# Kernel optimization log

Hardware: AMD Instinct MI355X
Metric: run time of the kernel (lower is better)

## Reference

```python
import jax, jax.numpy as jnp
import numpy as np

B, N_V, N_H, K = 16384, 4096, 1024, 3
LR, MOMENTUM, WEIGHT_DECAY = 1e-3, 0.5, 1e-4


def setup_inputs() -> dict:
    key = jax.random.key(0)
    k1, k2, k3, k4 = jax.random.split(key, 4)
    inputs = jax.random.uniform(k1, (B, N_V), dtype=jnp.float32)
    weights = jax.random.normal(k2, (N_V, N_H), dtype=jnp.float32) * 0.1
    visible_bias = jnp.ones((N_V,), jnp.float32) * 0.5
    hidden_bias = jnp.zeros((N_H,), jnp.float32)
    weights_momentum = jnp.zeros((N_V, N_H), jnp.float32)
    visible_bias_momentum = jnp.zeros((N_V,), jnp.float32)
    hidden_bias_momentum = jnp.zeros((N_H,), jnp.float32)
    # one uniform vector of length n_hidden per sampling step (matches torch code)
    rand_h0 = jax.random.uniform(k3, (N_H,), dtype=jnp.float32)
    rand_hk = jax.random.uniform(k4, (K, N_H), dtype=jnp.float32)
    return {
        "inputs": inputs,
        "weights": weights,
        "visible_bias": visible_bias,
        "hidden_bias": hidden_bias,
        "weights_momentum": weights_momentum,
        "visible_bias_momentum": visible_bias_momentum,
        "hidden_bias_momentum": hidden_bias_momentum,
        "rand_h0": rand_h0,
        "rand_hk": rand_hk,
    }


def reference(inputs, weights, visible_bias, hidden_bias,
              weights_momentum, visible_bias_momentum, hidden_bias_momentum,
              rand_h0, rand_hk):
    dtype = inputs.dtype

    def sample_hidden(v):  # [B,V] -> [B,H]
        return jax.nn.sigmoid(v @ weights + hidden_bias)

    def sample_visible(h):  # [B,H] -> [B,V]
        return jax.nn.sigmoid(h @ weights.T + visible_bias)

    # positive phase
    pos_hidden_probs = sample_hidden(inputs)                      # [B,H]
    pos_hidden_acts = (pos_hidden_probs >= rand_h0).astype(dtype)  # [B,H]
    pos_associations = inputs.T @ pos_hidden_acts                 # [V,H]

    # negative phase (CD-k). NOTE: in the original torch code `hid_acts` is
    # never updated inside the k-1 loop, so every iteration recomputes the
    # identical visible_probs/hidden_probs from pos_hidden_acts; the extra
    # bernoulli draws (rand_hk) only feed hidden_acts, which is discarded.
    # The final values are therefore exactly one reconstruction step:
    neg_visible_probs = sample_visible(pos_hidden_acts)           # [B,V]
    neg_hidden_probs = sample_hidden(neg_visible_probs)           # [B,H]
    neg_associations = neg_visible_probs.T @ neg_hidden_probs     # [V,H]

    # momentum optimizer step
    batch_size = inputs.shape[0]
    w_mom = weights_momentum * MOMENTUM + (pos_associations - neg_associations)
    vb_mom = visible_bias_momentum * MOMENTUM + jnp.sum(inputs - neg_visible_probs, axis=0)
    hb_mom = hidden_bias_momentum * MOMENTUM + jnp.sum(pos_hidden_probs - neg_hidden_probs, axis=0)

    new_weights = weights + w_mom * (LR / batch_size)
    new_weights = new_weights - new_weights * WEIGHT_DECAY
    new_visible_bias = visible_bias + vb_mom * (LR / batch_size)
    new_hidden_bias = hidden_bias + hb_mom * (LR / batch_size)

    # reconstruction error (original has a bug using builtin `input`; intended `inputs`)
    error = jnp.sum((inputs - neg_visible_probs) ** 2)
    return (error, new_weights, new_visible_bias, new_hidden_bias)
```

## Files before the change

kernel.cpp:

```cpp
#include <hip/hip_runtime.h>
#include <hip/hip_bf16.h>

#define DEV __device__ __forceinline__

typedef __attribute__((ext_vector_type(8))) short bhalf8;
typedef __attribute__((ext_vector_type(4))) short bhalf4;
typedef __attribute__((ext_vector_type(4))) float floatx4;
typedef unsigned short ushort_t;

constexpr int NB = 16384;
constexpr int NV = 4096;
constexpr int NH = 1024;
constexpr float MOM = 0.5f;
constexpr float WD  = 1e-4f;
constexpr float LRB = 1e-3f / 16384.0f;

constexpr int LDS_SHORTS = 65536;
constexpr size_t LDS_BYTES = 131136;

DEV unsigned short f2bf(float f) {
  unsigned u = __builtin_bit_cast(unsigned, f);
  u += 0x7FFFu + ((u >> 16) & 1u);
  return (unsigned short)(u >> 16);
}
DEV float bf2f(unsigned short u) {
  unsigned x = ((unsigned)u) << 16;
  return __builtin_bit_cast(float, x);
}
DEV float sigm(float x) { return 1.0f / (1.0f + __expf(-x)); }

DEV void gl16(const ushort_t* g, ushort_t* l) {
  __builtin_amdgcn_global_load_lds(
      (const __attribute__((address_space(1))) void*)g,
      (__attribute__((address_space(3))) void*)l,
      16, 0, 0);
}

__global__ void prep_cvt_t(const float* __restrict__ in,
                           ushort_t* __restrict__ obf,
                           ushort_t* __restrict__ oT, int R, int C) {
  __shared__ ushort_t t[64][72];
  const int c0 = blockIdx.x * 64, r0 = blockIdx.y * 64;
  const int tr = threadIdx.x >> 3, tc = (threadIdx.x & 7) * 8;
#pragma unroll
  for (int s = 0; s < 64; s += 32) {
    const float* p = in + (size_t)(r0 + tr + s) * C + c0 + tc;
    floatx4 lo = *(const floatx4*)p, hi = *(const floatx4*)(p + 4);
    bhalf8 r;
    r[0] = (short)f2bf(lo[0]); r[1] = (short)f2bf(lo[1]);
    r[2] = (short)f2bf(lo[2]); r[3] = (short)f2bf(lo[3]);
    r[4] = (short)f2bf(hi[0]); r[5] = (short)f2bf(hi[1]);
    r[6] = (short)f2bf(hi[2]); r[7] = (short)f2bf(hi[3]);
    *(bhalf8*)(obf + (size_t)(r0 + tr + s) * C + c0 + tc) = r;
    *(bhalf8*)&t[tr + s][tc] = r;
  }
  __syncthreads();
#pragma unroll
  for (int s = 0; s < 64; s += 32) {
    bhalf8 v;
#pragma unroll
    for (int j = 0; j < 8; ++j) v[j] = (short)t[tc + j][tr + s];
    *(bhalf8*)(oT + (size_t)(c0 + tr + s) * R + r0 + tc) = v;
  }
}

DEV void core256(const ushort_t* __restrict__ Ap,
                 const ushort_t* __restrict__ Bp,
                 size_t ldA, size_t ldB, int NP,
                 ushort_t* Lp, int wid, int lane,
                 int wr, int wc, floatx4 (&acc)[8][4]) {
  const int lr = lane & 15, kg = lane >> 4;
  const int srow = wid * 16 + (lane >> 2);
  const int scol = (lane & 3) * 8;
  const ushort_t* gA = Ap + (size_t)srow * ldA + scol;
  const ushort_t* gB = Bp + (size_t)srow * ldB + scol;
  ushort_t* dA = Lp + wid * 512;
  ushort_t* dB = Lp + 8192 + wid * 512;
  const ushort_t* aB = Lp + (wr * 128 + lr) * 32 + kg * 8;
  const ushort_t* bB = Lp + 8192 + (wc * 64 + lr) * 32 + kg * 8;

  auto stage = [&](int p) {
    const int slot = (p & 3) * 16384;
    const size_t kb = (size_t)p * 32;
#pragma unroll
    for (int i = 0; i < 2; ++i) {
      gl16(gA + (size_t)(i * 128) * ldA + kb, dA + slot + i * 4096);
      gl16(gB + (size_t)(i * 128) * ldB + kb, dB + slot + i * 4096);
    }
  };

  stage(0); stage(1); stage(2);
  asm volatile("s_waitcnt vmcnt(8)" ::: "memory");
  asm volatile("s_barrier" ::: "memory");

  for (int p = 0; p < NP; ++p) {
    const int slot = (p & 3) * 16384;
    bhalf8 fa[4], fb[4], fa2[4];
#pragma unroll
    for (int i = 0; i < 4; ++i) fa[i] = *(const bhalf8*)(aB + slot + i * 512);
#pragma unroll
    for (int i = 0; i < 4; ++i) fb[i] = *(const bhalf8*)(bB + slot + i * 512);
    if (p + 3 < NP) stage(p + 3);
    asm volatile("s_barrier" ::: "memory");
    asm volatile("s_waitcnt lgkmcnt(0)" ::: "memory");
    __builtin_amdgcn_sched_barrier(0);
    __builtin_amdgcn_s_setprio(1);
#pragma unroll
    for (int m2 = 0; m2 < 4; ++m2)
#pragma unroll
      for (int n = 0; n < 4; ++n)
        acc[m2][n] = __builtin_amdgcn_mfma_f32_16x16x32_bf16(fa[m2], fb[n], acc[m2][n], 0, 0, 0);
    __builtin_amdgcn_s_setprio(0);
    asm volatile("s_barrier" ::: "memory");
#pragma unroll
    for (int i = 0; i < 4; ++i) fa2[i] = *(const bhalf8*)(aB + slot + 2048 + i * 512);
    asm volatile("s_barrier" ::: "memory");
    asm volatile("s_waitcnt lgkmcnt(0)" ::: "memory");
    __builtin_amdgcn_sched_barrier(0);
    __builtin_amdgcn_s_setprio(1);
#pragma unroll
    for (int m2 = 0; m2 < 4; ++m2)
#pragma unroll
      for (int n = 0; n < 4; ++n)
        acc[4 + m2][n] = __builtin_amdgcn_mfma_f32_16x16x32_bf16(fa2[m2], fb[n], acc[4 + m2][n], 0, 0, 0);
    __builtin_amdgcn_s_setprio(0);
    if (p + 3 < NP)      asm volatile("s_waitcnt vmcnt(8)" ::: "memory");
    else if (p + 2 < NP) asm volatile("s_waitcnt vmcnt(4)" ::: "memory");
    else if (p + 1 < NP) asm volatile("s_waitcnt vmcnt(0)" ::: "memory");
    asm volatile("s_barrier" ::: "memory");
  }
}

template <int MODE>
__global__ __launch_bounds__(512, 2)
void gemm_fused256(const ushort_t* __restrict__ Ab,
                   const ushort_t* __restrict__ Bb,
                   int N, int K,
                   const float* __restrict__ bias,
                   const float* __restrict__ rand_h0,
                   ushort_t* __restrict__ Pout,
                   ushort_t* __restrict__ PoutT,
                   float* __restrict__ colsum,
                   const ushort_t* __restrict__ inbf,
                   float* __restrict__ err_accum) {
  extern __shared__ ushort_t Lsh[];
  const int tid = threadIdx.x;
  const int wid = tid >> 6, lane = tid & 63;
  const int wr = wid >> 2, wc = wid & 3;
  const int lr = lane & 15, kg = lane >> 4;

  const int nwg = gridDim.x * gridDim.y;
  const int id = blockIdx.y * gridDim.x + blockIdx.x;
  const int sid = (id & 7) * (nwg >> 3) + (id >> 3);
  const int n0 = (sid % gridDim.x) * 256;
  const int m0 = (sid / gridDim.x) * 256;

  floatx4 acc[8][4] = {};
  core256(Ab + (size_t)m0 * K, Bb + (size_t)n0 * K, K, K, K / 32,
          Lsh, wid, lane, wr, wc, acc);

  float esum = 0.0f;
#pragma unroll
  for (int ni = 0; ni < 4; ++ni) {
    const int col = n0 + wc * 64 + ni * 16 + lr;
    const float b = bias[col];
    const float r0 = (MODE == 0) ? rand_h0[col] : 0.0f;
    float cs = 0.0f;
#pragma unroll
    for (int mi = 0; mi < 8; ++mi) {
      const int rowb = m0 + wr * 128 + mi * 16 + kg * 4;
      bhalf4 tp;
#pragma unroll
      for (int r = 0; r < 4; ++r) {
        const float p = sigm(acc[mi][ni][r] + b);
        ushort_t ov;
        if (MODE == 0) {
          cs += p;
          ov = (p >= r0) ? (ushort_t)0x3F80u : (ushort_t)0u;
          Pout[(size_t)(rowb + r) * N + col] = ov;
        } else if (MODE == 1) {
          ov = f2bf(p);
          Pout[(size_t)(rowb + r) * N + col] = ov;
          const float d = bf2f(inbf[(size_t)(rowb + r) * N + col]) - p;
          cs += d;
          esum += d * d;
        } else {
          cs += p;
          ov = f2bf(p);
        }
        tp[r] = (short)ov;
      }
      *(bhalf4*)&PoutT[(size_t)col * NB + rowb] = tp;
    }
    cs += __shfl_xor(cs, 16);
    cs += __shfl_xor(cs, 32);
    if (kg == 0) atomicAdd(&colsum[col], cs);
  }
  if (MODE == 1) {
    float* ered = (float*)(Lsh + LDS_SHORTS);
    esum += __shfl_xor(esum, 1);
    esum += __shfl_xor(esum, 2);
    esum += __shfl_xor(esum, 4);
    esum += __shfl_xor(esum, 8);
    esum += __shfl_xor(esum, 16);
    esum += __shfl_xor(esum, 32);
    if (lane == 0) ered[wid] = esum;
    __syncthreads();
    if (tid == 0) {
      float s = 0.0f;
#pragma unroll
      for (int w = 0; w < 8; ++w) s += ered[w];
      atomicAdd(err_accum, s);
    }
  }
}

template <int EOP>
__global__ __launch_bounds__(512, 2)
void gemm_nt256(const ushort_t* __restrict__ Ab,
                const ushort_t* __restrict__ Bb,
                int Ng, int ld, int ksp, float* __restrict__ outd) {
  extern __shared__ ushort_t Lsh[];
  const int tid = threadIdx.x;
  const int wid = tid >> 6, lane = tid & 63;
  const int wr = wid >> 2, wc = wid & 3;
  const int lr = lane & 15, kg = lane >> 4;

  const int nwg = gridDim.x * gridDim.y;
  const int id = blockIdx.y * gridDim.x + blockIdx.x;
  const int sid = (id & 7) * (nwg >> 3) + (id >> 3);
  const int n0 = (sid % gridDim.x) * 256;
  const int m0 = (sid / gridDim.x) * 256;
  const size_t kb0 = (size_t)blockIdx.z * ksp;

  floatx4 acc[8][4] = {};
  core256(Ab + (size_t)m0 * ld + kb0, Bb + (size_t)n0 * ld + kb0, ld, ld, ksp / 32,
          Lsh, wid, lane, wr, wc, acc);

  float* od = outd + (size_t)blockIdx.z * (size_t)gridDim.y * 256 * Ng;
#pragma unroll
  for (int mi = 0; mi < 8; ++mi) {
    const int rowb = m0 + wr * 128 + mi * 16 + kg * 4;
#pragma unroll
    for (int ni = 0; ni < 4; ++ni) {
      const int col = n0 + wc * 64 + ni * 16 + lr;
#pragma unroll
      for (int r = 0; r < 4; ++r) {
        float* p = &od[(size_t)(rowb + r) * Ng + col];
        if (EOP == 0) *p = acc[mi][ni][r];
        else          *p -= acc[mi][ni][r];
      }
    }
  }
}

__global__ void wupdate_kernel(const float* __restrict__ W, const float* __restrict__ wm,
                               const float* __restrict__ diff, float* __restrict__ outW) {
  const int i = blockIdx.x * blockDim.x + threadIdx.x;
  constexpr size_t SL = (size_t)NV * NH / 4;
  const floatx4 w = ((const floatx4*)W)[i];
  const floatx4 m = ((const floatx4*)wm)[i];
  const floatx4 a = ((const floatx4*)diff)[i];
  const floatx4 b = ((const floatx4*)diff)[i + SL];
  const floatx4 c = ((const floatx4*)diff)[i + 2 * SL];
  const floatx4 d = ((const floatx4*)diff)[i + 3 * SL];
  floatx4 o;
#pragma unroll
  for (int j = 0; j < 4; ++j)
    o[j] = (w[j] + (m[j] * MOM + (a[j] + b[j]) + (c[j] + d[j])) * LRB) * (1.0f - WD);
  ((floatx4*)outW)[i] = o;
}

__global__ void biaserr_kernel(const float* __restrict__ vb, const float* __restrict__ vbm,
                               const float* __restrict__ vbcs,
                               const float* __restrict__ hb, const float* __restrict__ hbm,
                               const float* __restrict__ phpcs, const float* __restrict__ nhpcs,
                               const float* __restrict__ err, float* __restrict__ out) {
  const int i = blockIdx.x * blockDim.x + threadIdx.x;
  if (i < NV) out[1 + (size_t)NV * NH + i] = vb[i] + (vbm[i] * MOM + vbcs[i]) * LRB;
  if (i < NH) out[1 + (size_t)NV * NH + NV + i] = hb[i] + (hbm[i] * MOM + (phpcs[i] - nhpcs[i])) * LRB;
  if (i == 0) out[0] = err[0];
}

extern "C" void kernel_launch(void* const* d_in, const int* in_sizes, int n_in,
                              void* d_out, int out_size, void* d_ws, size_t ws_size,
                              hipStream_t stream) {
  const float* inputs  = (const float*)d_in[0];
  const float* W       = (const float*)d_in[1];
  const float* vb      = (const float*)d_in[2];
  const float* hb      = (const float*)d_in[3];
  const float* wmom    = (const float*)d_in[4];
  const float* vbmom   = (const float*)d_in[5];
  const float* hbmom   = (const float*)d_in[6];
  const float* rand_h0 = (const float*)d_in[7];

  hipFuncSetAttribute((const void*)gemm_fused256<0>, hipFuncAttributeMaxDynamicSharedMemorySize, (int)LDS_BYTES);
  hipFuncSetAttribute((const void*)gemm_fused256<1>, hipFuncAttributeMaxDynamicSharedMemorySize, (int)LDS_BYTES);
  hipFuncSetAttribute((const void*)gemm_fused256<2>, hipFuncAttributeMaxDynamicSharedMemorySize, (int)LDS_BYTES);
  hipFuncSetAttribute((const void*)gemm_nt256<0>, hipFuncAttributeMaxDynamicSharedMemorySize, (int)LDS_BYTES);
  hipFuncSetAttribute((const void*)gemm_nt256<1>, hipFuncAttributeMaxDynamicSharedMemorySize, (int)LDS_BYTES);

  char* ws = (char*)d_ws;
  size_t off = 0;
  auto take = [&](size_t b) { size_t r = off; off = (off + b + 1023) & ~(size_t)1023; return r; };
  ushort_t* Wbf   = (ushort_t*)(ws + take((size_t)NV * NH * 2));
  ushort_t* WT    = (ushort_t*)(ws + take((size_t)NV * NH * 2));
  ushort_t* inbf  = (ushort_t*)(ws + take((size_t)NB * NV * 2));
  ushort_t* inT   = (ushort_t*)(ws + take((size_t)NB * NV * 2));
  ushort_t* nvp   = (ushort_t*)(ws + take((size_t)NB * NV * 2));
  ushort_t* nvpT  = (ushort_t*)(ws + take((size_t)NB * NV * 2));
  ushort_t* acts  = (ushort_t*)(ws + take((size_t)NB * NH * 2));
  ushort_t* actsT = (ushort_t*)(ws + take((size_t)NB * NH * 2));
  ushort_t* nhpT  = (ushort_t*)(ws + take((size_t)NB * NH * 2));
  const size_t red_bytes = (size_t)(NH + NH + NV + 64) * 4;
  float* phpcs = (float*)(ws + take(red_bytes));
  float* nhpcs = phpcs + NH;
  float* vbcs  = nhpcs + NH;
  float* errp  = vbcs + NV;

  float* diff = (float*)inbf;

  hipMemsetAsync(phpcs, 0, red_bytes, stream);

  prep_cvt_t<<<dim3(NV / 64, NB / 64), 256, 0, stream>>>(inputs, inbf, inT, NB, NV);
  prep_cvt_t<<<dim3(NH / 64, NV / 64), 256, 0, stream>>>(W, Wbf, WT, NV, NH);

  gemm_fused256<0><<<dim3(NH / 256, NB / 256), 512, LDS_BYTES, stream>>>(
      inbf, WT, NH, NV, hb, rand_h0, acts, actsT, phpcs, nullptr, nullptr);

  gemm_fused256<1><<<dim3(NV / 256, NB / 256), 512, LDS_BYTES, stream>>>(
      acts, Wbf, NV, NH, vb, nullptr, nvp, nvpT, vbcs, inbf, errp);

  gemm_fused256<2><<<dim3(NH / 256, NB / 256), 512, LDS_BYTES, stream>>>(
      nvp, WT, NH, NV, hb, nullptr, nullptr, nhpT, nhpcs, nullptr, nullptr);

  gemm_nt256<0><<<dim3(NH / 256, NV / 256, 4), 512, LDS_BYTES, stream>>>(
      inT, actsT, NH, NB, NB / 4, diff);
  gemm_nt256<1><<<dim3(NH / 256, NV / 256, 4), 512, LDS_BYTES, stream>>>(
      nvpT, nhpT, NH, NB, NB / 4, diff);

  wupdate_kernel<<<dim3((NV * NH / 4) / 256), 256, 0, stream>>>(W, wmom, diff, (float*)d_out + 1);
  biaserr_kernel<<<dim3(16), 256, 0, stream>>>(vb, vbmom, vbcs, hb, hbmom, phpcs, nhpcs, errp,
                                               (float*)d_out);
}
```

Before: 1.152 ms.

## Shrink GEMM tiles to 256x128 with 4 waves, swizzled LDS, and fused dual NT GEMM

Replaces the 512-thread 256x256 GEMM core with a 256-thread 256x128 core. It uses a triple-buffered LDS pipeline with an XOR-swizzled layout to avoid bank conflicts and issues one barrier per k-step instead of four. The two split-K association GEMMs are merged into one kernel that accumulates pos minus neg in registers and writes each partial once, so the read-modify-write pass over the diff buffer goes away. LDS per block drops a lot, which allows more blocks per CU. In exchange each block gets less operand reuse, because B-tile loads are shared by fewer output columns.

```diff
diff --git a/kernel.cpp b/kernel.cpp
--- a/kernel.cpp
+++ b/kernel.cpp
@@ -15,8 +15,9 @@
 constexpr float WD  = 1e-4f;
 constexpr float LRB = 1e-3f / 16384.0f;
 
-constexpr int LDS_SHORTS = 65536;
-constexpr size_t LDS_BYTES = 131136;
+constexpr int BUF_SHORTS = 12288;
+constexpr int LDS_SHORTS = 3 * BUF_SHORTS;
+constexpr size_t LDS_BYTES = LDS_SHORTS * 2 + 64;
 
 DEV unsigned short f2bf(float f) {
   unsigned u = __builtin_bit_cast(unsigned, f);
@@ -64,75 +65,61 @@
   }
 }
 
-DEV void core256(const ushort_t* __restrict__ Ap,
-                 const ushort_t* __restrict__ Bp,
-                 size_t ldA, size_t ldB, int NP,
-                 ushort_t* Lp, int wid, int lane,
-                 int wr, int wc, floatx4 (&acc)[8][4]) {
+DEV void core(const ushort_t* __restrict__ Ap,
+              const ushort_t* __restrict__ Bp,
+              size_t ldA, size_t ldB, int nt,
+              ushort_t* Lp, int wid, int lane, int wm, int wn,
+              floatx4 (&acc)[8][4]) {
   const int lr = lane & 15, kg = lane >> 4;
-  const int srow = wid * 16 + (lane >> 2);
-  const int scol = (lane & 3) * 8;
-  const ushort_t* gA = Ap + (size_t)srow * ldA + scol;
-  const ushort_t* gB = Bp + (size_t)srow * ldB + scol;
-  ushort_t* dA = Lp + wid * 512;
-  ushort_t* dB = Lp + 8192 + wid * 512;
-  const ushort_t* aB = Lp + (wr * 128 + lr) * 32 + kg * 8;
-  const ushort_t* bB = Lp + 8192 + (wc * 64 + lr) * 32 + kg * 8;
-
-  auto stage = [&](int p) {
-    const int slot = (p & 3) * 16384;
-    const size_t kb = (size_t)p * 32;
-#pragma unroll
-    for (int i = 0; i < 2; ++i) {
-      gl16(gA + (size_t)(i * 128) * ldA + kb, dA + slot + i * 4096);
-      gl16(gB + (size_t)(i * 128) * ldB + kb, dB + slot + i * 4096);
-    }
+  const int sslot = ((lane & 3) ^ (((lane & 32) ? 2 : 0) | ((lane & 8) ? 1 : 0))) * 8;
+  const ushort_t* gA = Ap + (size_t)(wid * 16 + (lane >> 2)) * ldA + sslot;
+  const ushort_t* gB = Bp + (size_t)(wid * 16 + (lane >> 2)) * ldB + sslot;
+  const int rslot = ((kg ^ (((lr & 8) ? 2 : 0) | ((lr & 2) ? 1 : 0))) * 8);
+  const int aoff = (wm * 128 + lr) * 32 + rslot;
+  const int boff = 8192 + (wn * 64 + lr) * 32 + rslot;
+
+  auto stage = [&](int buf, int t) {
+    const ushort_t* a = gA + (size_t)t * 32;
+    const ushort_t* b = gB + (size_t)t * 32;
+    ushort_t* LA = Lp + buf * BUF_SHORTS + wid * 512;
+    ushort_t* LB = LA + 8192;
+#pragma unroll
+    for (int i = 0; i < 4; ++i) gl16(a + (size_t)(i * 64) * ldA, LA + i * 2048);
+#pragma unroll
+    for (int i = 0; i < 2; ++i) gl16(b + (size_t)(i * 64) * ldB, LB + i * 2048);
   };
 
-  stage(0); stage(1); stage(2);
-  asm volatile("s_waitcnt vmcnt(8)" ::: "memory");
-  asm volatile("s_barrier" ::: "memory");
-
-  for (int p = 0; p < NP; ++p) {
-    const int slot = (p & 3) * 16384;
-    bhalf8 fa[4], fb[4], fa2[4];
-#pragma unroll
-    for (int i = 0; i < 4; ++i) fa[i] = *(const bhalf8*)(aB + slot + i * 512);
-#pragma unroll
-    for (int i = 0; i < 4; ++i) fb[i] = *(const bhalf8*)(bB + slot + i * 512);
-    if (p + 3 < NP) stage(p + 3);
+  stage(0, 0);
+  stage(1, 1);
+  int cur = 0, pre = 2;
+  for (int t = 0; t < nt; ++t) {
+    if (t + 1 < nt) asm volatile("s_waitcnt vmcnt(6)" ::: "memory");
+    else            asm volatile("s_waitcnt vmcnt(0)" ::: "memory");
     asm volatile("s_barrier" ::: "memory");
+    if (t + 2 < nt) stage(pre, t + 2);
+    const ushort_t* aB = Lp + cur * BUF_SHORTS + aoff;
+    const ushort_t* bB = Lp + cur * BUF_SHORTS + boff;
+    bhalf8 fa[8], fb[4];
+#pragma unroll
+    for (int m = 0; m < 8; ++m) fa[m] = *(const bhalf8*)(aB + m * 512);
+#pragma unroll
+    for (int n = 0; n < 4; ++n) fb[n] = *(const bhalf8*)(bB + n * 512);
     asm volatile("s_waitcnt lgkmcnt(0)" ::: "memory");
     __builtin_amdgcn_sched_barrier(0);
     __builtin_amdgcn_s_setprio(1);
 #pragma unroll
-    for (int m2 = 0; m2 < 4; ++m2)
+    for (int m = 0; m < 8; ++m)
 #pragma unroll
       for (int n = 0; n < 4; ++n)
-        acc[m2][n] = __builtin_amdgcn_mfma_f32_16x16x32_bf16(fa[m2], fb[n], acc[m2][n], 0, 0, 0);
+        acc[m][n] = __builtin_amdgcn_mfma_f32_16x16x32_bf16(fa[m], fb[n], acc[m][n], 0, 0, 0);
     __builtin_amdgcn_s_setprio(0);
-    asm volatile("s_barrier" ::: "memory");
-#pragma unroll
-    for (int i = 0; i < 4; ++i) fa2[i] = *(const bhalf8*)(aB + slot + 2048 + i * 512);
-    asm volatile("s_barrier" ::: "memory");
-    asm volatile("s_waitcnt lgkmcnt(0)" ::: "memory");
-    __builtin_amdgcn_sched_barrier(0);
-    __builtin_amdgcn_s_setprio(1);
-#pragma unroll
-    for (int m2 = 0; m2 < 4; ++m2)
-#pragma unroll
-      for (int n = 0; n < 4; ++n)
-        acc[4 + m2][n] = __builtin_amdgcn_mfma_f32_16x16x32_bf16(fa2[m2], fb[n], acc[4 + m2][n], 0, 0, 0);
-    __builtin_amdgcn_s_setprio(0);
-    if (p + 3 < NP)      asm volatile("s_waitcnt vmcnt(8)" ::: "memory");
-    else if (p + 2 < NP) asm volatile("s_waitcnt vmcnt(4)" ::: "memory");
-    else if (p + 1 < NP) asm volatile("s_waitcnt vmcnt(0)" ::: "memory");
-    asm volatile("s_barrier" ::: "memory");
+    if (++cur == 3) cur = 0;
+    if (++pre == 3) pre = 0;
   }
 }
 
 template <int MODE>
-__global__ __launch_bounds__(512, 2)
+__global__ __launch_bounds__(256, 2)
 void gemm_fused256(const ushort_t* __restrict__ Ab,
                    const ushort_t* __restrict__ Bb,
                    int N, int K,
@@ -146,29 +133,29 @@
   extern __shared__ ushort_t Lsh[];
   const int tid = threadIdx.x;
   const int wid = tid >> 6, lane = tid & 63;
-  const int wr = wid >> 2, wc = wid & 3;
+  const int wm = wid >> 1, wn = wid & 1;
   const int lr = lane & 15, kg = lane >> 4;
 
   const int nwg = gridDim.x * gridDim.y;
   const int id = blockIdx.y * gridDim.x + blockIdx.x;
   const int sid = (id & 7) * (nwg >> 3) + (id >> 3);
-  const int n0 = (sid % gridDim.x) * 256;
+  const int n0 = (sid % gridDim.x) * 128;
   const int m0 = (sid / gridDim.x) * 256;
 
   floatx4 acc[8][4] = {};
-  core256(Ab + (size_t)m0 * K, Bb + (size_t)n0 * K, K, K, K / 32,
-          Lsh, wid, lane, wr, wc, acc);
+  core(Ab + (size_t)m0 * K, Bb + (size_t)n0 * K, K, K, K / 32,
+       Lsh, wid, lane, wm, wn, acc);
 
   float esum = 0.0f;
 #pragma unroll
   for (int ni = 0; ni < 4; ++ni) {
-    const int col = n0 + wc * 64 + ni * 16 + lr;
+    const int col = n0 + wn * 64 + ni * 16 + lr;
     const float b = bias[col];
     const float r0 = (MODE == 0) ? rand_h0[col] : 0.0f;
     float cs = 0.0f;
 #pragma unroll
     for (int mi = 0; mi < 8; ++mi) {
-      const int rowb = m0 + wr * 128 + mi * 16 + kg * 4;
+      const int rowb = m0 + wm * 128 + mi * 16 + kg * 4;
       bhalf4 tp;
 #pragma unroll
       for (int r = 0; r < 4; ++r) {
@@ -204,52 +191,52 @@
     esum += __shfl_xor(esum, 8);
     esum += __shfl_xor(esum, 16);
     esum += __shfl_xor(esum, 32);
+    __syncthreads();
     if (lane == 0) ered[wid] = esum;
     __syncthreads();
-    if (tid == 0) {
-      float s = 0.0f;
-#pragma unroll
-      for (int w = 0; w < 8; ++w) s += ered[w];
-      atomicAdd(err_accum, s);
-    }
-  }
-}
-
-template <int EOP>
-__global__ __launch_bounds__(512, 2)
-void gemm_nt256(const ushort_t* __restrict__ Ab,
-                const ushort_t* __restrict__ Bb,
-                int Ng, int ld, int ksp, float* __restrict__ outd) {
+    if (tid == 0) atomicAdd(err_accum, ered[0] + ered[1] + ered[2] + ered[3]);
+  }
+}
+
+__global__ __launch_bounds__(256, 2)
+void gemm_nt_dual(const ushort_t* __restrict__ A1, const ushort_t* __restrict__ B1,
+                  const ushort_t* __restrict__ A2, const ushort_t* __restrict__ B2,
+                  float* __restrict__ outd) {
   extern __shared__ ushort_t Lsh[];
   const int tid = threadIdx.x;
   const int wid = tid >> 6, lane = tid & 63;
-  const int wr = wid >> 2, wc = wid & 3;
+  const int wm = wid >> 1, wn = wid & 1;
   const int lr = lane & 15, kg = lane >> 4;
 
-  const int nwg = gridDim.x * gridDim.y;
-  const int id = blockIdx.y * gridDim.x + blockIdx.x;
-  const int sid = (id & 7) * (nwg >> 3) + (id >> 3);
-  const int n0 = (sid % gridDim.x) * 256;
-  const int m0 = (sid / gridDim.x) * 256;
-  const size_t kb0 = (size_t)blockIdx.z * ksp;
+  const int bid = blockIdx.x;
+  const int r = bid & 127;
+  const int m0 = (r & 15) * 256;
+  const int n0 = (r >> 4) * 128;
+  const int z  = bid >> 7;
+  const size_t kb0 = (size_t)z * (NB / 4);
+  constexpr int NT = (NB / 4) / 32;
 
   floatx4 acc[8][4] = {};
-  core256(Ab + (size_t)m0 * ld + kb0, Bb + (size_t)n0 * ld + kb0, ld, ld, ksp / 32,
-          Lsh, wid, lane, wr, wc, acc);
-
-  float* od = outd + (size_t)blockIdx.z * (size_t)gridDim.y * 256 * Ng;
+  core(A1 + (size_t)m0 * NB + kb0, B1 + (size_t)n0 * NB + kb0, NB, NB, NT,
+       Lsh, wid, lane, wm, wn, acc);
+#pragma unroll
+  for (int m = 0; m < 8; ++m)
+#pragma unroll
+    for (int n = 0; n < 4; ++n)
+#pragma unroll
+      for (int j = 0; j < 4; ++j) acc[m][n][j] = -acc[m][n][j];
+  core(A2 + (size_t)m0 * NB + kb0, B2 + (size_t)n0 * NB + kb0, NB, NB, NT,
+       Lsh, wid, lane, wm, wn, acc);
+  float* od = outd + (size_t)z * NV * NH;
 #pragma unroll
   for (int mi = 0; mi < 8; ++mi) {
-    const int rowb = m0 + wr * 128 + mi * 16 + kg * 4;
+    const int rowb = m0 + wm * 128 + mi * 16 + kg * 4;
 #pragma unroll
     for (int ni = 0; ni < 4; ++ni) {
-      const int col = n0 + wc * 64 + ni * 16 + lr;
-#pragma unroll
-      for (int r = 0; r < 4; ++r) {
-        float* p = &od[(size_t)(rowb + r) * Ng + col];
-        if (EOP == 0) *p = acc[mi][ni][r];
-        else          *p -= acc[mi][ni][r];
-      }
+      const int col = n0 + wn * 64 + ni * 16 + lr;
+#pragma unroll
+      for (int r2 = 0; r2 < 4; ++r2)
+        od[(size_t)(rowb + r2) * NH + col] = -acc[mi][ni][r2];
     }
   }
 }
@@ -297,8 +284,7 @@
   hipFuncSetAttribute((const void*)gemm_fused256<0>, hipFuncAttributeMaxDynamicSharedMemorySize, (int)LDS_BYTES);
   hipFuncSetAttribute((const void*)gemm_fused256<1>, hipFuncAttributeMaxDynamicSharedMemorySize, (int)LDS_BYTES);
   hipFuncSetAttribute((const void*)gemm_fused256<2>, hipFuncAttributeMaxDynamicSharedMemorySize, (int)LDS_BYTES);
-  hipFuncSetAttribute((const void*)gemm_nt256<0>, hipFuncAttributeMaxDynamicSharedMemorySize, (int)LDS_BYTES);
-  hipFuncSetAttribute((const void*)gemm_nt256<1>, hipFuncAttributeMaxDynamicSharedMemorySize, (int)LDS_BYTES);
+  hipFuncSetAttribute((const void*)gemm_nt_dual, hipFuncAttributeMaxDynamicSharedMemorySize, (int)LDS_BYTES);
 
   char* ws = (char*)d_ws;
   size_t off = 0;
@@ -325,19 +311,16 @@
   prep_cvt_t<<<dim3(NV / 64, NB / 64), 256, 0, stream>>>(inputs, inbf, inT, NB, NV);
   prep_cvt_t<<<dim3(NH / 64, NV / 64), 256, 0, stream>>>(W, Wbf, WT, NV, NH);
 
-  gemm_fused256<0><<<dim3(NH / 256, NB / 256), 512, LDS_BYTES, stream>>>(
+  gemm_fused256<0><<<dim3(NH / 128, NB / 256), 256, LDS_BYTES, stream>>>(
       inbf, WT, NH, NV, hb, rand_h0, acts, actsT, phpcs, nullptr, nullptr);
 
-  gemm_fused256<1><<<dim3(NV / 256, NB / 256), 512, LDS_BYTES, stream>>>(
+  gemm_fused256<1><<<dim3(NV / 128, NB / 256), 256, LDS_BYTES, stream>>>(
       acts, Wbf, NV, NH, vb, nullptr, nvp, nvpT, vbcs, inbf, errp);
 
-  gemm_fused256<2><<<dim3(NH / 256, NB / 256), 512, LDS_BYTES, stream>>>(
+  gemm_fused256<2><<<dim3(NH / 128, NB / 256), 256, LDS_BYTES, stream>>>(
       nvp, WT, NH, NV, hb, nullptr, nullptr, nhpT, nhpcs, nullptr, nullptr);
 
-  gemm_nt256<0><<<dim3(NH / 256, NV / 256, 4), 512, LDS_BYTES, stream>>>(
-      inT, actsT, NH, NB, NB / 4, diff);
-  gemm_nt256<1><<<dim3(NH / 256, NV / 256, 4), 512, LDS_BYTES, stream>>>(
-      nvpT, nhpT, NH, NB, NB / 4, diff);
+  gemm_nt_dual<<<dim3(512), 256, LDS_BYTES, stream>>>(inT, actsT, nvpT, nhpT, diff);
 
   wupdate_kernel<<<dim3((NV * NH / 4) / 256), 256, 0, stream>>>(W, wmom, diff, (float*)d_out + 1);
   biaserr_kernel<<<dim3(16), 256, 0, stream>>>(vb, vbmom, vbcs, hb, hbmom, phpcs, nhpcs, errp,
```

Result: no change. 1.143 ms (-0.8%).
